# Kernel optimization log

Hardware: AMD Instinct MI355X
Metric: run time of the kernel (lower is better)

Reference implementation:

```python
import jax, jax.numpy as jnp
import numpy as np
import math

D_MODEL = 1024
H = 16
D_K = D_MODEL // H
B = 4
S = 2048
NEG = -1e9


def setup_inputs() -> dict:
    key = jax.random.key(0)
    ks = jax.random.split(key, 11)
    scale = 1.0 / math.sqrt(D_MODEL)
    inp = {
        'q': jax.random.normal(ks[0], (B, S, D_MODEL), dtype=jnp.float32),
        'k': jax.random.normal(ks[1], (B, S, D_MODEL), dtype=jnp.float32),
        'v': jax.random.normal(ks[2], (B, S, D_MODEL), dtype=jnp.float32),
        'wq': jax.random.normal(ks[3], (D_MODEL, D_MODEL), dtype=jnp.float32) * scale,
        'bq': jnp.zeros((D_MODEL,), dtype=jnp.float32),
        'wk': jax.random.normal(ks[4], (D_MODEL, D_MODEL), dtype=jnp.float32) * scale,
        'bk': jnp.zeros((D_MODEL,), dtype=jnp.float32),
        'wv': jax.random.normal(ks[5], (D_MODEL, D_MODEL), dtype=jnp.float32) * scale,
        'bv': jnp.zeros((D_MODEL,), dtype=jnp.float32),
        'wo': jax.random.normal(ks[6], (D_MODEL, D_MODEL), dtype=jnp.float32) * scale,
        'bo': jnp.zeros((D_MODEL,), dtype=jnp.float32),
        # broadcastable causal mask [1, 1, S, S]; 0 = masked out
        'mask': jnp.tril(jnp.ones((S, S), dtype=jnp.int32))[None, None, :, :],
    }
    return inp


def reference(q, k, v, wq, bq, wk, bk, wv, bv, wo, bo, mask):
    # QKV projections: x @ W^T + b (nn.Linear convention)
    def split_heads(x):  # [B, S, D] -> [B, H, S, d_k]
        return x.reshape(B, S, H, D_K).transpose(0, 2, 1, 3)

    query = split_heads(q @ wq.T + bq)
    key_ = split_heads(k @ wk.T + bk)
    value = split_heads(v @ wv.T + bv)

    # scaled dot-product attention with mask; scores: [B, H, S, S]
    scores = jnp.einsum('bhqd,bhkd->bhqk', query, key_) / math.sqrt(D_K)
    scores = jnp.where(mask == 0, jnp.float32(NEG), scores)
    attn = jax.nn.softmax(scores, axis=-1)
    ctx = jnp.einsum('bhqk,bhkd->bhqd', attn, value)  # [B, H, S, d_k]

    # merge heads and output projection
    ctx = ctx.transpose(0, 2, 1, 3).reshape(B, S, D_MODEL)
    return ctx @ wo.T + bo
```

## Files before the change

### kernel.cpp

```cpp
#include <hip/hip_runtime.h>

#define DEVI __device__ __forceinline__

typedef __attribute__((ext_vector_type(8))) __bf16 bf16x8;
typedef __attribute__((ext_vector_type(4))) float f32x4;
typedef __attribute__((ext_vector_type(16))) float f32x16;
typedef __attribute__((ext_vector_type(4))) unsigned uint32x4;

DEVI __bf16 f2bf(float f) {
  unsigned u = __builtin_bit_cast(unsigned, f);
  unsigned r = u + 0x7fffu + ((u >> 16) & 1u);
  unsigned short h = (unsigned short)(r >> 16);
  return __builtin_bit_cast(__bf16, h);
}

DEVI unsigned cvt_pk_bf16(float lo, float hi) {
  unsigned r;
  asm("v_cvt_pk_bf16_f32 %0, %1, %2" : "=v"(r) : "v"(lo), "v"(hi));
  return r;
}

DEVI void load_lds16(const void* g, void* l) {
  __builtin_amdgcn_global_load_lds((__attribute__((address_space(1))) const void*)g,
                                   (__attribute__((address_space(3))) void*)l,
                                   16, 0, 0);
}

__global__ void convert_bf16(const float* __restrict__ in, __bf16* __restrict__ out, int n8) {
  int stride = gridDim.x * blockDim.x;
  for (int i = blockIdx.x * blockDim.x + threadIdx.x; i < n8; i += stride) {
    float4 a = ((const float4*)in)[i * 2];
    float4 b = ((const float4*)in)[i * 2 + 1];
    bf16x8 o;
    o[0] = f2bf(a.x); o[1] = f2bf(a.y); o[2] = f2bf(a.z); o[3] = f2bf(a.w);
    o[4] = f2bf(b.x); o[5] = f2bf(b.y); o[6] = f2bf(b.z); o[7] = f2bf(b.w);
    ((bf16x8*)out)[i] = o;
  }
}

template<int MODE>
__global__ __launch_bounds__(256, 2) void gemm_bt(
    const __bf16* __restrict__ A, const __bf16* __restrict__ W,
    const float* __restrict__ bias, void* __restrict__ outp)
{
  __shared__ __bf16 As[2][128 * 32];
  __shared__ __bf16 Bs[2][128 * 32];
  const int tid = threadIdx.x;
  const int lane = tid & 63;
  const int ln = lane & 15, g = lane >> 4;
  const int w = tid >> 6;
  const int wr = w >> 1, wc = w & 1;
  const int id = blockIdx.y * 64 + blockIdx.x;
  const int bx = 8 * (id & 7) + ((id >> 3) & 7);
  const int by = id >> 6;
  const int row0 = bx * 128, col0 = by * 128;

  f32x4 acc[4][4] = {};

  auto stage = [&](int buf, int k0) {
#pragma unroll
    for (int i = 0; i < 2; ++i) {
      int c = tid + 256 * i;
      int r = c >> 2, ko = (c & 3) * 8;
      load_lds16(&A[(size_t)(row0 + r) * 1024 + k0 + ko], &As[buf][c * 8]);
      load_lds16(&W[(size_t)(col0 + r) * 1024 + k0 + ko], &Bs[buf][c * 8]);
    }
  };

  stage(0, 0);
#pragma unroll 2
  for (int kt = 0; kt < 32; ++kt) {
    __syncthreads();
    if (kt + 1 < 32) stage((kt + 1) & 1, (kt + 1) * 32);
    const __bf16* as = As[kt & 1];
    const __bf16* bs = Bs[kt & 1];
    bf16x8 aF[4], bF[4];
#pragma unroll
    for (int mi = 0; mi < 4; ++mi)
      aF[mi] = *(const bf16x8*)&as[(wr * 64 + mi * 16 + ln) * 32 + g * 8];
#pragma unroll
    for (int ni = 0; ni < 4; ++ni)
      bF[ni] = *(const bf16x8*)&bs[(wc * 64 + ni * 16 + ln) * 32 + g * 8];
    __builtin_amdgcn_s_setprio(1);
#pragma unroll
    for (int mi = 0; mi < 4; ++mi)
#pragma unroll
      for (int ni = 0; ni < 4; ++ni)
        acc[mi][ni] = __builtin_amdgcn_mfma_f32_16x16x32_bf16(aF[mi], bF[ni], acc[mi][ni], 0, 0, 0);
    __builtin_amdgcn_s_setprio(0);
  }

#pragma unroll
  for (int ni = 0; ni < 4; ++ni) {
    int n = col0 + wc * 64 + ni * 16 + ln;
    float bv = bias[n];
#pragma unroll
    for (int mi = 0; mi < 4; ++mi) {
#pragma unroll
      for (int i = 0; i < 4; ++i) {
        int m = row0 + wr * 64 + mi * 16 + g * 4 + i;
        float val = acc[mi][ni][i] + bv;
        if (MODE == 2) {
          ((float*)outp)[(size_t)m * 1024 + n] = val;
        } else {
          int b = m >> 11, s = m & 2047, h = n >> 6, d = n & 63;
          size_t idx = (MODE == 0)
            ? ((size_t)((b * 16 + h) * 2048 + s) * 64 + d)
            : ((size_t)((b * 16 + h) * 64 + d) * 2048 + s);
          ((__bf16*)outp)[idx] = f2bf(val);
        }
      }
    }
  }
}

__global__ __launch_bounds__(512, 4) void attn_fwd(
    const __bf16* __restrict__ Qh, const __bf16* __restrict__ Kh,
    const __bf16* __restrict__ Vt, __bf16* __restrict__ Ctx)
{
  __shared__ __bf16 KVs[8][64 * 64];

  const int tid = threadIdx.x;
  const int lane = tid & 63;
  const int l31 = lane & 31, hl = lane >> 5;
  const int w = tid >> 6;
  const int wq3 = w & 3, p = w >> 2;
  const int bh = blockIdx.x;
  const int b = bh >> 4, h = bh & 15;
  const float CE = 0.18033688f;
  const float MC = 40.0f * CE;

  auto stagePair = [&](int tp) {
    const int base = 2 * (tp & 1);
    const int c = tid;
    const int r = c >> 3, sl = c & 7;
    const int so = 8 * (sl ^ (r & 7));
#pragma unroll
    for (int i = 0; i < 2; ++i) {
      const int kv0 = (2 * tp + i) * 64, s = base + i;
      load_lds16(&Kh[((size_t)bh * 2048 + kv0 + r) * 64 + so], &KVs[s][c * 8]);
      load_lds16(&Vt[((size_t)bh * 64 + r) * 2048 + kv0 + so], &KVs[4 + s][c * 8]);
    }
  };

  auto strip = [&](int qb) {
    const int q0 = qb * 128;
    const int qw = q0 + wq3 * 32;
    const int qglob = qw + l31;
    const int np = qb + 1;

    bf16x8 qF[4];
#pragma unroll
    for (int ds = 0; ds < 4; ++ds)
      qF[ds] = *(const bf16x8*)&Qh[((size_t)bh * 2048 + qglob) * 64 + ds * 16 + hl * 8];

    f32x16 oT[2] = {};
    float lrun = 0.f;

    __syncthreads();
    stagePair(0);
    for (int tp = 0; tp < np; ++tp) {
      __syncthreads();
      if (tp + 1 < np) stagePair(tp + 1);
      const int kv0 = (2 * tp + p) * 64;
      if (kv0 > qw + 31) continue;
      const __bf16* ksm = KVs[2 * (tp & 1) + p];
      const __bf16* vsm = KVs[4 + 2 * (tp & 1) + p];

      f32x16 sT[2] = {};
#pragma unroll
      for (int kblk = 0; kblk < 2; ++kblk) {
        bf16x8 aK[4];
        const int r = kblk * 32 + l31;
#pragma unroll
        for (int ds = 0; ds < 4; ++ds)
          aK[ds] = *(const bf16x8*)&ksm[r * 64 + ((ds * 16 + hl * 8) ^ ((r & 7) * 8))];
        __builtin_amdgcn_s_setprio(1);
#pragma unroll
        for (int ds = 0; ds < 4; ++ds)
          sT[kblk] = __builtin_amdgcn_mfma_f32_32x32x16_bf16(aK[ds], qF[ds], sT[kblk], 0, 0, 0);
        __builtin_amdgcn_s_setprio(0);
      }

      if (kv0 + 63 > qw) {
#pragma unroll
        for (int kblk = 0; kblk < 2; ++kblk)
#pragma unroll
          for (int r = 0; r < 16; ++r) {
            int kvg = kv0 + kblk * 32 + (r & 3) + 8 * (r >> 2) + 4 * hl;
            sT[kblk][r] = (kvg <= qglob) ? sT[kblk][r] : -3e38f;
          }
      }

      unsigned c0[8], c1[8];
      float ps0 = 0.f, ps1 = 0.f, ps2 = 0.f, ps3 = 0.f;
#pragma unroll
      for (int w2 = 0; w2 < 8; ++w2) {
        float p0 = exp2f(__builtin_fmaf(sT[0][2 * w2],     CE, -MC));
        float p1 = exp2f(__builtin_fmaf(sT[0][2 * w2 + 1], CE, -MC));
        float p2 = exp2f(__builtin_fmaf(sT[1][2 * w2],     CE, -MC));
        float p3 = exp2f(__builtin_fmaf(sT[1][2 * w2 + 1], CE, -MC));
        ps0 += p0; ps1 += p1; ps2 += p2; ps3 += p3;
        c0[w2] = cvt_pk_bf16(p0, p1);
        c1[w2] = cvt_pk_bf16(p2, p3);
      }
      lrun += (ps0 + ps1) + (ps2 + ps3);

      uint32x4 Wv[4];
#pragma unroll
      for (int kblk = 0; kblk < 2; ++kblk)
#pragma unroll
        for (int ksl = 0; ksl < 2; ++ksl)
#pragma unroll
          for (int al = 0; al < 2; ++al) {
            unsigned cp = kblk ? c1[4 * ksl + al]     : c0[4 * ksl + al];
            unsigned cq = kblk ? c1[4 * ksl + 2 + al] : c0[4 * ksl + 2 + al];
            unsigned cqx = __shfl_xor(cq, 32);
            unsigned cpx = __shfl_xor(cp, 32);
            Wv[kblk * 2 + ksl][al]     = hl ? cqx : cp;
            Wv[kblk * 2 + ksl][al + 2] = hl ? cq  : cpx;
          }

#pragma unroll
      for (int dblk = 0; dblk < 2; ++dblk) {
        bf16x8 aV[4];
        const int r = dblk * 32 + l31;
#pragma unroll
        for (int ks = 0; ks < 4; ++ks)
          aV[ks] = *(const bf16x8*)&vsm[r * 64 + ((ks * 16 + hl * 8) ^ ((r & 7) * 8))];
        __builtin_amdgcn_s_setprio(1);
#pragma unroll
        for (int ks = 0; ks < 4; ++ks)
          oT[dblk] = __builtin_amdgcn_mfma_f32_32x32x16_bf16(
              aV[ks], __builtin_bit_cast(bf16x8, Wv[ks]), oT[dblk], 0, 0, 0);
        __builtin_amdgcn_s_setprio(0);
      }
    }

    __syncthreads();
    float* ex = (float*)KVs + wq3 * 2176 + lane * 34;
    if (p == 1) {
      lrun += __shfl_xor(lrun, 32);
#pragma unroll
      for (int dblk = 0; dblk < 2; ++dblk)
#pragma unroll
        for (int rb = 0; rb < 8; ++rb)
          *(float2*)(ex + dblk * 16 + rb * 2) =
              make_float2(oT[dblk][2 * rb], oT[dblk][2 * rb + 1]);
      ex[32] = lrun;
    }
    __syncthreads();
    if (p == 0) {
      lrun += __shfl_xor(lrun, 32);
      lrun += ex[32];
#pragma unroll
      for (int dblk = 0; dblk < 2; ++dblk)
#pragma unroll
        for (int rb = 0; rb < 8; ++rb) {
          float2 v = *(float2*)(ex + dblk * 16 + rb * 2);
          oT[dblk][2 * rb]     += v.x;
          oT[dblk][2 * rb + 1] += v.y;
        }
      const float inv = 1.0f / fmaxf(lrun, 1e-30f);
#pragma unroll
      for (int dblk = 0; dblk < 2; ++dblk)
#pragma unroll
        for (int rb = 0; rb < 4; ++rb) {
          unsigned u0 = cvt_pk_bf16(oT[dblk][4 * rb]     * inv, oT[dblk][4 * rb + 1] * inv);
          unsigned u1 = cvt_pk_bf16(oT[dblk][4 * rb + 2] * inv, oT[dblk][4 * rb + 3] * inv);
          int d = dblk * 32 + rb * 8 + 4 * hl;
          size_t idx = ((size_t)(b * 2048 + qglob)) * 1024 + h * 64 + d;
          *(uint2*)&Ctx[idx] = make_uint2(u0, u1);
        }
    }
  };

  strip(15 - (int)blockIdx.y);
  strip((int)blockIdx.y);
}

extern "C" void kernel_launch(void* const* d_in, const int* in_sizes, int n_in,
                              void* d_out, int out_size, void* d_ws, size_t ws_size,
                              hipStream_t stream) {
  const float* q  = (const float*)d_in[0];
  const float* k  = (const float*)d_in[1];
  const float* v  = (const float*)d_in[2];
  const float* wq = (const float*)d_in[3];
  const float* bq = (const float*)d_in[4];
  const float* wk = (const float*)d_in[5];
  const float* bk = (const float*)d_in[6];
  const float* wv = (const float*)d_in[7];
  const float* bv = (const float*)d_in[8];
  const float* wo = (const float*)d_in[9];
  const float* bo = (const float*)d_in[10];
  float* out = (float*)d_out;
  char* ws = (char*)d_ws;

  const size_t MB = 1024 * 1024;
  __bf16* Wqb  = (__bf16*)(ws + 0 * MB);
  __bf16* Wkb  = (__bf16*)(ws + 2 * MB);
  __bf16* Wvb  = (__bf16*)(ws + 4 * MB);
  __bf16* Wob  = (__bf16*)(ws + 6 * MB);
  __bf16* Abuf = (__bf16*)(ws + 8 * MB);
  __bf16* Qh   = (__bf16*)(ws + 24 * MB);
  __bf16* Kh   = (__bf16*)(ws + 40 * MB);
  __bf16* Vt   = (__bf16*)(ws + 56 * MB);
  __bf16* Ctx  = Abuf;

  const int W8 = 1024 * 1024 / 8;
  const int X8 = 8192 * 1024 / 8;
  auto cgrid = [](int n8) { int nb = (n8 + 255) / 256; return dim3((unsigned)(nb < 2048 ? nb : 2048)); };

  convert_bf16<<<cgrid(W8), 256, 0, stream>>>(wq, Wqb, W8);
  convert_bf16<<<cgrid(W8), 256, 0, stream>>>(wk, Wkb, W8);
  convert_bf16<<<cgrid(W8), 256, 0, stream>>>(wv, Wvb, W8);
  convert_bf16<<<cgrid(W8), 256, 0, stream>>>(wo, Wob, W8);

  dim3 ggrid(64, 8);
  convert_bf16<<<cgrid(X8), 256, 0, stream>>>(q, Abuf, X8);
  gemm_bt<0><<<ggrid, 256, 0, stream>>>(Abuf, Wqb, bq, Qh);
  convert_bf16<<<cgrid(X8), 256, 0, stream>>>(k, Abuf, X8);
  gemm_bt<0><<<ggrid, 256, 0, stream>>>(Abuf, Wkb, bk, Kh);
  convert_bf16<<<cgrid(X8), 256, 0, stream>>>(v, Abuf, X8);
  gemm_bt<1><<<ggrid, 256, 0, stream>>>(Abuf, Wvb, bv, Vt);

  attn_fwd<<<dim3(64, 8), 512, 0, stream>>>(Qh, Kh, Vt, Ctx);
  gemm_bt<2><<<ggrid, 256, 0, stream>>>(Ctx, Wob, bo, out);
}
```

Before: 211.8 us.

## Triple-buffer GEMM staging with XOR-swizzled LDS and batch weight conversions

The projection GEMM moves from double to triple buffering in LDS. Each iteration now waits with vmcnt(4) and a raw barrier, so loads run two tiles ahead and are hidden behind MFMA work. The LDS layout is XOR-swizzled across 16-byte slots to reduce bank conflicts on the fragment reads. The four weight conversion launches are merged into one kernel to cut launch overhead. The cost is more LDS per block, which may reduce occupancy, plus more fragile manual waitcnt handling.

Result: faster. 205.0 us (-3.2%).

```diff
diff --git a/kernel.cpp b/kernel.cpp
--- a/kernel.cpp
+++ b/kernel.cpp
@@ -38,13 +38,31 @@
   }
 }
 
+__global__ void convert_w4(const float* __restrict__ w0, const float* __restrict__ w1,
+                           const float* __restrict__ w2, const float* __restrict__ w3,
+                           __bf16* __restrict__ o0, __bf16* __restrict__ o1,
+                           __bf16* __restrict__ o2, __bf16* __restrict__ o3, int n8) {
+  int stride = gridDim.x * blockDim.x;
+  for (int i = blockIdx.x * blockDim.x + threadIdx.x; i < 4 * n8; i += stride) {
+    int sel = i / n8, j = i - sel * n8;
+    const float* in = sel == 0 ? w0 : sel == 1 ? w1 : sel == 2 ? w2 : w3;
+    __bf16* out = sel == 0 ? o0 : sel == 1 ? o1 : sel == 2 ? o2 : o3;
+    float4 a = ((const float4*)in)[j * 2];
+    float4 b = ((const float4*)in)[j * 2 + 1];
+    bf16x8 o;
+    o[0] = f2bf(a.x); o[1] = f2bf(a.y); o[2] = f2bf(a.z); o[3] = f2bf(a.w);
+    o[4] = f2bf(b.x); o[5] = f2bf(b.y); o[6] = f2bf(b.z); o[7] = f2bf(b.w);
+    ((bf16x8*)out)[j] = o;
+  }
+}
+
 template<int MODE>
 __global__ __launch_bounds__(256, 2) void gemm_bt(
     const __bf16* __restrict__ A, const __bf16* __restrict__ W,
     const float* __restrict__ bias, void* __restrict__ outp)
 {
-  __shared__ __bf16 As[2][128 * 32];
-  __shared__ __bf16 Bs[2][128 * 32];
+  __shared__ __bf16 As[3][128 * 32];
+  __shared__ __bf16 Bs[3][128 * 32];
   const int tid = threadIdx.x;
   const int lane = tid & 63;
   const int ln = lane & 15, g = lane >> 4;
@@ -57,30 +75,32 @@
 
   f32x4 acc[4][4] = {};
 
-  auto stage = [&](int buf, int k0) {
+  auto stage = [&](int buf, int kt) {
+    const int k0 = kt * 32;
 #pragma unroll
     for (int i = 0; i < 2; ++i) {
       int c = tid + 256 * i;
-      int r = c >> 2, ko = (c & 3) * 8;
-      load_lds16(&A[(size_t)(row0 + r) * 1024 + k0 + ko], &As[buf][c * 8]);
-      load_lds16(&W[(size_t)(col0 + r) * 1024 + k0 + ko], &Bs[buf][c * 8]);
+      int r = c >> 2, sl = c & 3;
+      int so = 8 * (sl ^ ((r >> 1) & 3));
+      load_lds16(&A[(size_t)(row0 + r) * 1024 + k0 + so], &As[buf][c * 8]);
+      load_lds16(&W[(size_t)(col0 + r) * 1024 + k0 + so], &Bs[buf][c * 8]);
     }
   };
 
-  stage(0, 0);
-#pragma unroll 2
-  for (int kt = 0; kt < 32; ++kt) {
-    __syncthreads();
-    if (kt + 1 < 32) stage((kt + 1) & 1, (kt + 1) * 32);
-    const __bf16* as = As[kt & 1];
-    const __bf16* bs = Bs[kt & 1];
+  auto compute = [&](int buf) {
+    const __bf16* as = As[buf];
+    const __bf16* bs = Bs[buf];
     bf16x8 aF[4], bF[4];
 #pragma unroll
-    for (int mi = 0; mi < 4; ++mi)
-      aF[mi] = *(const bf16x8*)&as[(wr * 64 + mi * 16 + ln) * 32 + g * 8];
-#pragma unroll
-    for (int ni = 0; ni < 4; ++ni)
-      bF[ni] = *(const bf16x8*)&bs[(wc * 64 + ni * 16 + ln) * 32 + g * 8];
+    for (int mi = 0; mi < 4; ++mi) {
+      int r = wr * 64 + mi * 16 + ln;
+      aF[mi] = *(const bf16x8*)&as[r * 32 + ((g * 8) ^ (((r >> 1) & 3) * 8))];
+    }
+#pragma unroll
+    for (int ni = 0; ni < 4; ++ni) {
+      int r = wc * 64 + ni * 16 + ln;
+      bF[ni] = *(const bf16x8*)&bs[r * 32 + ((g * 8) ^ (((r >> 1) & 3) * 8))];
+    }
     __builtin_amdgcn_s_setprio(1);
 #pragma unroll
     for (int mi = 0; mi < 4; ++mi)
@@ -88,7 +108,22 @@
       for (int ni = 0; ni < 4; ++ni)
         acc[mi][ni] = __builtin_amdgcn_mfma_f32_16x16x32_bf16(aF[mi], bF[ni], acc[mi][ni], 0, 0, 0);
     __builtin_amdgcn_s_setprio(0);
+  };
+
+  stage(0, 0);
+  stage(1, 1);
+#pragma unroll 1
+  for (int kt = 0; kt < 31; ++kt) {
+    asm volatile("s_waitcnt vmcnt(4)" ::: "memory");
+    __builtin_amdgcn_s_barrier();
+    asm volatile("" ::: "memory");
+    if (kt + 2 < 32) stage((kt + 2) % 3, kt + 2);
+    compute(kt % 3);
   }
+  asm volatile("s_waitcnt vmcnt(0)" ::: "memory");
+  __builtin_amdgcn_s_barrier();
+  asm volatile("" ::: "memory");
+  compute(31 % 3);
 
 #pragma unroll
   for (int ni = 0; ni < 4; ++ni) {
@@ -311,10 +346,7 @@
   const int X8 = 8192 * 1024 / 8;
   auto cgrid = [](int n8) { int nb = (n8 + 255) / 256; return dim3((unsigned)(nb < 2048 ? nb : 2048)); };
 
-  convert_bf16<<<cgrid(W8), 256, 0, stream>>>(wq, Wqb, W8);
-  convert_bf16<<<cgrid(W8), 256, 0, stream>>>(wk, Wkb, W8);
-  convert_bf16<<<cgrid(W8), 256, 0, stream>>>(wv, Wvb, W8);
-  convert_bf16<<<cgrid(W8), 256, 0, stream>>>(wo, Wob, W8);
+  convert_w4<<<2048, 256, 0, stream>>>(wq, wk, wv, wo, Wqb, Wkb, Wvb, Wob, W8);
 
   dim3 ggrid(64, 8);
   convert_bf16<<<cgrid(X8), 256, 0, stream>>>(q, Abuf, X8);
```
